# Performance work log

Measured on AMD Instinct MI355X. Metric: run time of the kernel, lower is better.

The kernel has to match this reference:

```python
import jax, jax.numpy as jnp
import numpy as np
from jax import lax

NPOL = 125   # polar grid size (hardcoded in module)
NANG = 126   # number of correlation offsets / angle bins


def polar_grid(n=NPOL):
    # u in [0, sqrt(2)], v in [-pi, pi]; torch.meshgrid default is 'ij'
    u = jnp.linspace(0.0, np.sqrt(2.0), n)
    v = jnp.linspace(-np.pi, np.pi, n)
    vs, us = jnp.meshgrid(v, u, indexing='ij')
    return jnp.stack([us * jnp.cos(vs), us * jnp.sin(vs)], axis=-1)  # (n, n, 2)


def grid_sample(img, grid):
    """Bilinear grid_sample, align_corners=True, zero padding.
    img: [B,C,H,W], grid: [B,Hg,Wg,2] (x,y) normalized coords. -> [B,C,Hg,Wg]"""
    B, C, H, W = img.shape
    ix = (grid[..., 0] + 1.0) * 0.5 * (W - 1)
    iy = (grid[..., 1] + 1.0) * 0.5 * (H - 1)
    x0 = jnp.floor(ix); y0 = jnp.floor(iy)
    x1 = x0 + 1.0; y1 = y0 + 1.0
    bidx = jnp.arange(B)[:, None, None]

    def corner(yc, xc, w):
        valid = (xc >= 0) & (xc <= W - 1) & (yc >= 0) & (yc <= H - 1)
        xi = jnp.clip(xc, 0, W - 1).astype(jnp.int32)
        yi = jnp.clip(yc, 0, H - 1).astype(jnp.int32)
        val = img[bidx, :, yi, xi]                 # [B,Hg,Wg,C]
        return val * (w * valid)[..., None]

    out = (corner(y0, x0, (x1 - ix) * (y1 - iy))
           + corner(y0, x1, (ix - x0) * (y1 - iy))
           + corner(y1, x0, (x1 - ix) * (iy - y0))
           + corner(y1, x1, (ix - x0) * (iy - y0)))
    return out.transpose(0, 3, 1, 2)


def affine_grid(mat, n=NPOL):
    # F.affine_grid align_corners=True over (n, n) output
    xs = jnp.linspace(-1.0, 1.0, n)
    yy, xx = jnp.meshgrid(xs, xs, indexing='ij')
    base = jnp.stack([xx, yy, jnp.ones_like(xx)], axis=-1)  # [n,n,3]
    return jnp.einsum('bij,hwj->bhwi', mat, base)           # [B,n,n,2]


def setup_inputs() -> dict:
    key = jax.random.key(0)
    k1, k2 = jax.random.split(key)
    Embd1 = jax.random.normal(k1, (32, 64, 128, 128), dtype=jnp.float32)
    Embd2 = jax.random.normal(k2, (32, 64, 128, 128), dtype=jnp.float32)
    return {"Embd1": Embd1, "Embd2": Embd2}


def reference(Embd1, Embd2):
    B, C, H, W = Embd1.shape
    pgrid = jnp.broadcast_to(polar_grid(), (B, NPOL, NPOL, 2))
    P1 = grid_sample(Embd1, pgrid)                 # [B,C,125,125]
    P2 = grid_sample(Embd2, pgrid)                 # [B,C,125,125]
    # torch.flip(input1, [1, 0]) flips channel AND batch dims (faithful)
    translated = jnp.flip(P1, axis=(0, 1))
    aug = jnp.concatenate([P1, translated], axis=2)  # [B,C,250,125]
    # per-sample full cross-correlation as grouped conv: 126 vertical offsets
    corr = lax.conv_general_dilated(
        aug.reshape(1, B * C, 2 * NPOL, NPOL), P2,
        window_strides=(1, 1), padding='VALID',
        dimension_numbers=('NCHW', 'OIHW', 'NCHW'),
        feature_group_count=B)                     # [1,B,126,1]
    scores = corr[0, :, :, 0]                      # [B,126]
    angles = jnp.linspace(-np.pi, np.pi, NANG)
    p = jax.nn.softmax(scores, axis=-1)
    theta = jnp.sum(p * angles, axis=-1) - np.pi   # [B]
    c, s = jnp.cos(theta), jnp.sin(theta)
    z = jnp.zeros_like(c)
    Mat = jnp.stack([jnp.stack([c, -s, z], axis=-1),
                     jnp.stack([s, c, z], axis=-1)], axis=1)  # [B,2,3]
    img_transform = grid_sample(Embd1, affine_grid(Mat))       # [B,C,125,125]
    return img_transform, Mat
```

## Files before the change

### kernel.cpp

```cpp
#include <hip/hip_runtime.h>
#include <math.h>
#include <stdint.h>

#define NPOL 125
#define NANG 126
#define BB 32
#define CC 64
#define HH 128
#define WW 128
#define PIX (NPOL*NPOL)
#define PI_F 3.14159265358979323846f

typedef __attribute__((ext_vector_type(4))) float f32x4;
typedef _Float16 f16x8 __attribute__((ext_vector_type(8)));
union U16 { uint4 u; f16x8 v; };

__global__ __launch_bounds__(256) void kz_zero(float* __restrict__ p, int n) {
    int i = blockIdx.x * 256 + threadIdx.x;
    if (i < n) p[i] = 0.0f;
}

__device__ __forceinline__ float bil(const float* __restrict__ img, float u, float cv, float sv) {
    float x = u * cv, y = u * sv;
    float ix = (x + 1.0f) * 0.5f * 127.0f;
    float iy = (y + 1.0f) * 0.5f * 127.0f;
    float x0 = floorf(ix), y0 = floorf(iy);
    float wx1 = ix - x0, wy1 = iy - y0;
    float wx0 = 1.0f - wx1, wy0 = 1.0f - wy1;
    float mx0 = (x0 >= 0.0f && x0 <= 127.0f) ? wx0 : 0.0f;
    float mx1 = (x0 >= -1.0f && x0 <= 126.0f) ? wx1 : 0.0f;
    float my0 = (y0 >= 0.0f && y0 <= 127.0f) ? wy0 : 0.0f;
    float my1 = (y0 >= -1.0f && y0 <= 126.0f) ? wy1 : 0.0f;
    int xi0 = (int)fminf(fmaxf(x0, 0.0f), 127.0f);
    int xi1 = (int)fminf(fmaxf(x0 + 1.0f, 0.0f), 127.0f);
    int yi0 = (int)fminf(fmaxf(y0, 0.0f), 127.0f);
    int yi1 = (int)fminf(fmaxf(y0 + 1.0f, 0.0f), 127.0f);
    return my0 * (mx0 * img[yi0 * WW + xi0] + mx1 * img[yi0 * WW + xi1])
         + my1 * (mx0 * img[yi1 * WW + xi0] + mx1 * img[yi1 * WW + xi1]);
}

__global__ __launch_bounds__(512, 2) void k2_fused(const float* __restrict__ E1,
                                                   const float* __restrict__ E2,
                                                   double* __restrict__ scores) {
    __shared__ unsigned bufA[16384];
    __shared__ unsigned bufB[16384];
    __shared__ float tabU[128];
    __shared__ float tabC[128];
    __shared__ float tabS[128];
    __shared__ double sd[2][NANG];

    const int tid  = threadIdx.x;
    const int lane = tid & 63;
    const int wid  = tid >> 6;
    const int wm   = wid >> 2;
    const int wn   = wid & 3;
    const int frow = lane & 15;
    const int kq   = lane >> 4;

    const int bp = blockIdx.x & 15;
    const int kg = blockIdx.x >> 4;

    if (tid < 128) {
        double dj = (double)tid;
        tabU[tid] = (tid < NPOL) ? (float)(dj * (1.4142135623730951 / 124.0)) : 0.0f;
        double v  = -3.14159265358979323846 + dj * (6.28318530717958647692 / 124.0);
        tabC[tid] = (tid < NPOL) ? (float)cos(v) : 0.0f;
        tabS[tid] = (tid < NPOL) ? (float)sin(v) : 0.0f;
    }
    if (tid < 2 * NANG) ((double*)sd)[tid] = 0.0;

    f32x4 acc0[4][2], acc1[4][2], acc2[4][2], acc3[4][2];
    #pragma unroll
    for (int mi = 0; mi < 4; ++mi)
        #pragma unroll
        for (int ni = 0; ni < 2; ++ni) {
            acc0[mi][ni] = (f32x4){0.f,0.f,0.f,0.f};
            acc1[mi][ni] = (f32x4){0.f,0.f,0.f,0.f};
            acc2[mi][ni] = (f32x4){0.f,0.f,0.f,0.f};
            acc3[mi][ni] = (f32x4){0.f,0.f,0.f,0.f};
        }

    float4 stg[8];
    unsigned hw[16], lw[16];

    {
        const float4* p0 = (const float4*)(E1 + (size_t)(bp * CC + kg * 4) * (HH * WW));
        #pragma unroll
        for (int k = 0; k < 8; ++k) stg[k] = p0[k * 512 + tid];
    }

#define LOADPLANE(BUF, NEXTP) do {                                              \
    _Pragma("unroll")                                                           \
    for (int k_ = 0; k_ < 8; ++k_) ((float4*)(BUF))[k_ * 512 + tid] = stg[k_];  \
    __syncthreads();                                                            \
    if (NEXTP) {                                                                \
        const float4* np_ = (const float4*)(NEXTP);                             \
        _Pragma("unroll")                                                       \
        for (int k_ = 0; k_ < 8; ++k_) stg[k_] = np_[k_ * 512 + tid];           \
    }                                                                           \
    {                                                                           \
        const float* f_ = (const float*)(BUF);                                  \
        _Pragma("unroll")                                                       \
        for (int it_ = 0; it_ < 16; ++it_) {                                    \
            int s_ = tid + it_ * 512;                                           \
            if (s_ < 8000) {                                                    \
                int r_ = s_ >> 6, p_ = s_ & 63;                                 \
                float cv_ = tabC[r_], sv_ = tabS[r_];                           \
                int j0_ = 2 * p_, j1_ = 2 * p_ + 1;                             \
                float va_ = bil(f_, tabU[j0_], cv_, sv_);                       \
                float vb_ = bil(f_, tabU[j1_], cv_, sv_);                       \
                if (j0_ >= NPOL) va_ = 0.0f;                                    \
                if (j1_ >= NPOL) vb_ = 0.0f;                                    \
                _Float16 h0_ = (_Float16)va_;                                   \
                _Float16 h1_ = (_Float16)vb_;                                   \
                _Float16 l0_ = (_Float16)(va_ - (float)h0_);                    \
                _Float16 l1_ = (_Float16)(vb_ - (float)h1_);                    \
                hw[it_] = (unsigned)__builtin_bit_cast(unsigned short, h0_)     \
                        | ((unsigned)__builtin_bit_cast(unsigned short, h1_) << 16); \
                lw[it_] = (unsigned)__builtin_bit_cast(unsigned short, l0_)     \
                        | ((unsigned)__builtin_bit_cast(unsigned short, l1_) << 16); \
            }                                                                   \
        }                                                                       \
    }                                                                           \
    __syncthreads();                                                            \
    _Pragma("unroll")                                                           \
    for (int it_ = 0; it_ < 16; ++it_) {                                        \
        int s_ = tid + it_ * 512;                                               \
        if (s_ < 8000) {                                                        \
            int r_ = s_ >> 6, p_ = s_ & 63;                                     \
            int ih_ = (r_ * 128 + p_) ^ ((r_ & 7) << 2);                        \
            (BUF)[ih_]      = hw[it_];                                          \
            (BUF)[ih_ + 64] = lw[it_];                                          \
        }                                                                       \
    }                                                                           \
    if (tid < 384) {                                                            \
        int rr_ = 125 + (tid >> 7), pp_ = tid & 127;                            \
        (BUF)[rr_ * 128 + pp_] = 0u;                                            \
    }                                                                           \
    __syncthreads();                                                            \
} while (0)

#define MPHASE(ACC) do {                                                        \
    _Pragma("unroll")                                                           \
    for (int jc_ = 0; jc_ < 4; ++jc_) {                                         \
        U16 ah_[4], al_[4], bh_[2], bl_[2];                                     \
        _Pragma("unroll")                                                       \
        for (int ni_ = 0; ni_ < 2; ++ni_) {                                     \
            int row_ = wn * 32 + ni_ * 16 + frow;                               \
            int idx_ = (row_ * 128 + jc_ * 16 + kq * 4) ^ ((row_ & 7) << 2);    \
            bh_[ni_].u = *(const uint4*)(bufB + idx_);                          \
            bl_[ni_].u = *(const uint4*)(bufB + idx_ + 64);                     \
        }                                                                       \
        _Pragma("unroll")                                                       \
        for (int mi_ = 0; mi_ < 4; ++mi_) {                                     \
            int row_ = wm * 64 + mi_ * 16 + frow;                               \
            int idx_ = (row_ * 128 + jc_ * 16 + kq * 4) ^ ((row_ & 7) << 2);    \
            ah_[mi_].u = *(const uint4*)(bufA + idx_);                          \
            al_[mi_].u = *(const uint4*)(bufA + idx_ + 64);                     \
        }                                                                       \
        _Pragma("unroll")                                                       \
        for (int mi_ = 0; mi_ < 4; ++mi_)                                       \
            _Pragma("unroll")                                                   \
            for (int ni_ = 0; ni_ < 2; ++ni_) {                                 \
                ACC[mi_][ni_] = __builtin_amdgcn_mfma_f32_16x16x32_f16(ah_[mi_].v, bh_[ni_].v, ACC[mi_][ni_], 0, 0, 0); \
                ACC[mi_][ni_] = __builtin_amdgcn_mfma_f32_16x16x32_f16(ah_[mi_].v, bl_[ni_].v, ACC[mi_][ni_], 0, 0, 0); \
                ACC[mi_][ni_] = __builtin_amdgcn_mfma_f32_16x16x32_f16(al_[mi_].v, bh_[ni_].v, ACC[mi_][ni_], 0, 0, 0); \
            }                                                                   \
    }                                                                           \
} while (0)

    for (int cl = 0; cl < 4; ++cl) {
        const int c  = kg * 4 + cl;
        const int cb = 63 - c;
        const float* pA1 = E1 + (size_t)(bp * CC + c) * (HH * WW);
        const float* pA2 = E1 + (size_t)((31 - bp) * CC + cb) * (HH * WW);
        const float* pB1 = E2 + (size_t)(bp * CC + c) * (HH * WW);
        const float* pB2 = E2 + (size_t)((31 - bp) * CC + cb) * (HH * WW);
        const float* pNx = (cl < 3) ? (pA1 + HH * WW) : nullptr;

        LOADPLANE(bufA, pB1);
        LOADPLANE(bufB, pA2);
        MPHASE(acc0);
        __syncthreads();
        LOADPLANE(bufA, pB2);
        MPHASE(acc1);
        __syncthreads();
        LOADPLANE(bufB, pA1);
        MPHASE(acc2);
        __syncthreads();
        LOADPLANE(bufA, pNx);
        MPHASE(acc3);
        __syncthreads();
    }

#define EPI(ACC, SDI, TOFF) do {                                                \
    float part_[5][4];                                                          \
    _Pragma("unroll")                                                           \
    for (int d_ = 0; d_ < 5; ++d_)                                              \
        _Pragma("unroll")                                                       \
        for (int r_ = 0; r_ < 4; ++r_) part_[d_][r_] = 0.0f;                    \
    _Pragma("unroll")                                                           \
    for (int mi_ = 0; mi_ < 4; ++mi_)                                           \
        _Pragma("unroll")                                                       \
        for (int ni_ = 0; ni_ < 2; ++ni_) {                                     \
            int d_ = mi_ - ni_ + 1;                                             \
            _Pragma("unroll")                                                   \
            for (int r_ = 0; r_ < 4; ++r_) part_[d_][r_] += ACC[mi_][ni_][r_];  \
        }                                                                       \
    int tb_ = (TOFF) + wm * 64 - wn * 32 + ((lane >> 4) << 2) - (lane & 15);    \
    _Pragma("unroll")                                                           \
    for (int d_ = 0; d_ < 5; ++d_)                                              \
        _Pragma("unroll")                                                       \
        for (int r_ = 0; r_ < 4; ++r_) {                                        \
            int t_ = tb_ + (d_ - 1) * 16 + r_;                                  \
            if (t_ >= 0 && t_ < NANG) atomicAdd(&sd[SDI][t_], (double)part_[d_][r_]); \
        }                                                                       \
} while (0)

    EPI(acc0, 0, 0);
    EPI(acc1, 0, 125);
    EPI(acc2, 1, 0);
    EPI(acc3, 1, 125);
    __syncthreads();
    if (tid < 2 * NANG) {
        int o = (tid < NANG) ? 0 : 1;
        int t = tid - o * NANG;
        int b = o ? (31 - bp) : bp;
        atomicAdd(&scores[b * NANG + t], sd[o][t]);
    }
#undef LOADPLANE
#undef MPHASE
#undef EPI
}

__global__ __launch_bounds__(128) void k3_theta(const double* __restrict__ scores, float* __restrict__ matOut) {
    const int b = blockIdx.x;
    const int t = threadIdx.x;
    __shared__ double sd[128];
    __shared__ double red[128];

    double sval = (t < NANG) ? scores[b * NANG + t] : -1e300;
    sd[t]  = sval;
    red[t] = sval;
    __syncthreads();
    for (int st = 64; st > 0; st >>= 1) {
        if (t < st) red[t] = fmax(red[t], red[t + st]);
        __syncthreads();
    }
    const double m = red[0];
    __syncthreads();
    const double e = (t < NANG) ? exp(sd[t] - m) : 0.0;
    red[t] = e;
    __syncthreads();
    for (int st = 64; st > 0; st >>= 1) {
        if (t < st) red[t] += red[t + st];
        __syncthreads();
    }
    const double Z = red[0];
    __syncthreads();
    const double ang = -3.14159265358979323846 + (double)t * (6.28318530717958647692 / 125.0);
    red[t] = e * ang;
    __syncthreads();
    for (int st = 64; st > 0; st >>= 1) {
        if (t < st) red[t] += red[t + st];
        __syncthreads();
    }
    if (t == 0) {
        double theta = red[0] / Z - 3.14159265358979323846;
        float cth = (float)cos(theta), sth = (float)sin(theta);
        float* M = matOut + b * 6;
        M[0] = cth; M[1] = -sth; M[2] = 0.0f;
        M[3] = sth; M[4] = cth;  M[5] = 0.0f;
    }
}

__global__ __launch_bounds__(512) void k4_affine(const float* __restrict__ img, const float* __restrict__ mat,
                                                 float* __restrict__ out) {
    __shared__ float plane[HH * WW];
    const int bc  = blockIdx.x;
    const int b   = bc >> 6;
    const int tid = threadIdx.x;
    const float4* src = (const float4*)img + (size_t)bc * (HH * WW / 4);
    float4* d4 = (float4*)plane;
    #pragma unroll
    for (int it = 0; it < 8; ++it) d4[it * 512 + tid] = src[it * 512 + tid];
    __syncthreads();
    const float M0 = mat[b * 6 + 0], M1 = mat[b * 6 + 1];
    const float M3 = mat[b * 6 + 3], M4 = mat[b * 6 + 4];
    const int base = bc * PIX;
    for (int pix = tid; pix < PIX; pix += 512) {
        int i = pix / NPOL;
        int j = pix - i * NPOL;
        float xx = (float)(-1.0 + (double)j * (2.0 / 124.0));
        float yy = (float)(-1.0 + (double)i * (2.0 / 124.0));
        float gx = M0 * xx + M1 * yy;
        float gy = M3 * xx + M4 * yy;
        float ix = (gx + 1.0f) * 0.5f * 127.0f;
        float iy = (gy + 1.0f) * 0.5f * 127.0f;
        float x0 = floorf(ix), y0 = floorf(iy);
        float wx1 = ix - x0, wy1 = iy - y0;
        float wx0 = 1.0f - wx1, wy0 = 1.0f - wy1;
        float mx0 = (x0 >= 0.0f && x0 <= 127.0f) ? wx0 : 0.0f;
        float mx1 = (x0 >= -1.0f && x0 <= 126.0f) ? wx1 : 0.0f;
        float my0 = (y0 >= 0.0f && y0 <= 127.0f) ? wy0 : 0.0f;
        float my1 = (y0 >= -1.0f && y0 <= 126.0f) ? wy1 : 0.0f;
        int xi0 = (int)fminf(fmaxf(x0, 0.0f), 127.0f);
        int xi1 = (int)fminf(fmaxf(x0 + 1.0f, 0.0f), 127.0f);
        int yi0 = (int)fminf(fmaxf(y0, 0.0f), 127.0f);
        int yi1 = (int)fminf(fmaxf(y0 + 1.0f, 0.0f), 127.0f);
        float val = my0 * (mx0 * plane[yi0 * WW + xi0] + mx1 * plane[yi0 * WW + xi1])
                  + my1 * (mx0 * plane[yi1 * WW + xi0] + mx1 * plane[yi1 * WW + xi1]);
        out[base + pix] = val;
    }
}

extern "C" void kernel_launch(void* const* d_in, const int* in_sizes, int n_in,
                              void* d_out, int out_size, void* d_ws, size_t ws_size,
                              hipStream_t stream) {
    const float* E1 = (const float*)d_in[0];
    const float* E2 = (const float*)d_in[1];
    float*  out    = (float*)d_out;
    float*  matOut = out + 32000000;
    double* scores = (double*)d_ws;

    kz_zero<<<(2 * BB * NANG + 255) / 256, 256, 0, stream>>>((float*)scores, 2 * BB * NANG);
    k2_fused<<<256, 512, 0, stream>>>(E1, E2, scores);
    k3_theta<<<BB, 128, 0, stream>>>(scores, matOut);
    k4_affine<<<BB * CC, 512, 0, stream>>>(E1, matOut, out);
}
```

Baseline: 420.0 us.

## Stage input planes with direct global-to-LDS loads instead of register prefetch

Replaces the register-staged prefetch, where the next plane was held in float4 registers while the current one was converted, with `global_load_lds` copies straight into shared memory. The load, convert and MFMA phases are reordered so each plane is staged, a barrier is taken, and then it is converted in place. The MFMA loop also loads A fragments one at a time instead of as a four-entry array. This frees many VGPRs, which may help occupancy and scheduling, but the next plane's global load no longer overlaps the current conversion, so load latency may be exposed at each barrier.

After: 621.9 us. +48.1%, slower.

```diff
diff --git a/kernel.cpp b/kernel.cpp
--- a/kernel.cpp
+++ b/kernel.cpp
@@ -18,6 +18,13 @@
 __global__ __launch_bounds__(256) void kz_zero(float* __restrict__ p, int n) {
     int i = blockIdx.x * 256 + threadIdx.x;
     if (i < n) p[i] = 0.0f;
+}
+
+__device__ __forceinline__ void gload16(const float* g, unsigned* l) {
+    __builtin_amdgcn_global_load_lds(
+        (const __attribute__((address_space(1))) void*)g,
+        (__attribute__((address_space(3))) void*)l,
+        16, 0, 0);
 }
 
 __device__ __forceinline__ float bil(const float* __restrict__ img, float u, float cv, float sv) {
@@ -80,46 +87,36 @@
             acc3[mi][ni] = (f32x4){0.f,0.f,0.f,0.f};
         }
 
-    float4 stg[8];
-    unsigned hw[16], lw[16];
-
-    {
-        const float4* p0 = (const float4*)(E1 + (size_t)(bp * CC + kg * 4) * (HH * WW));
-        #pragma unroll
-        for (int k = 0; k < 8; ++k) stg[k] = p0[k * 512 + tid];
-    }
-
-#define LOADPLANE(BUF, NEXTP) do {                                              \
-    _Pragma("unroll")                                                           \
-    for (int k_ = 0; k_ < 8; ++k_) ((float4*)(BUF))[k_ * 512 + tid] = stg[k_];  \
-    __syncthreads();                                                            \
-    if (NEXTP) {                                                                \
-        const float4* np_ = (const float4*)(NEXTP);                             \
-        _Pragma("unroll")                                                       \
-        for (int k_ = 0; k_ < 8; ++k_) stg[k_] = np_[k_ * 512 + tid];           \
-    }                                                                           \
-    {                                                                           \
-        const float* f_ = (const float*)(BUF);                                  \
-        _Pragma("unroll")                                                       \
-        for (int it_ = 0; it_ < 16; ++it_) {                                    \
-            int s_ = tid + it_ * 512;                                           \
-            if (s_ < 8000) {                                                    \
-                int r_ = s_ >> 6, p_ = s_ & 63;                                 \
-                float cv_ = tabC[r_], sv_ = tabS[r_];                           \
-                int j0_ = 2 * p_, j1_ = 2 * p_ + 1;                             \
-                float va_ = bil(f_, tabU[j0_], cv_, sv_);                       \
-                float vb_ = bil(f_, tabU[j1_], cv_, sv_);                       \
-                if (j0_ >= NPOL) va_ = 0.0f;                                    \
-                if (j1_ >= NPOL) vb_ = 0.0f;                                    \
-                _Float16 h0_ = (_Float16)va_;                                   \
-                _Float16 h1_ = (_Float16)vb_;                                   \
-                _Float16 l0_ = (_Float16)(va_ - (float)h0_);                    \
-                _Float16 l1_ = (_Float16)(vb_ - (float)h1_);                    \
-                hw[it_] = (unsigned)__builtin_bit_cast(unsigned short, h0_)     \
-                        | ((unsigned)__builtin_bit_cast(unsigned short, h1_) << 16); \
-                lw[it_] = (unsigned)__builtin_bit_cast(unsigned short, l0_)     \
-                        | ((unsigned)__builtin_bit_cast(unsigned short, l1_) << 16); \
-            }                                                                   \
+#define STAGE(BUF, PTR) do {                                                    \
+    const float* g_ = (PTR) + wid * 256 + lane * 4;                             \
+    unsigned* l_ = (BUF) + wid * 256;                                           \
+    _Pragma("unroll")                                                           \
+    for (int r_ = 0; r_ < 8; ++r_)                                              \
+        gload16(g_ + r_ * 2048, l_ + r_ * 2048);                                \
+} while (0)
+
+#define CONVERT(BUF) do {                                                       \
+    const float* f_ = (const float*)(BUF);                                      \
+    unsigned hw_[16], lw_[16];                                                  \
+    _Pragma("unroll")                                                           \
+    for (int it_ = 0; it_ < 16; ++it_) {                                        \
+        int s_ = tid + it_ * 512;                                               \
+        if (s_ < 8000) {                                                        \
+            int r_ = s_ >> 6, p_ = s_ & 63;                                     \
+            float cv_ = tabC[r_], sv_ = tabS[r_];                               \
+            int j0_ = 2 * p_, j1_ = 2 * p_ + 1;                                 \
+            float va_ = bil(f_, tabU[j0_], cv_, sv_);                           \
+            float vb_ = bil(f_, tabU[j1_], cv_, sv_);                           \
+            if (j0_ >= NPOL) va_ = 0.0f;                                        \
+            if (j1_ >= NPOL) vb_ = 0.0f;                                        \
+            _Float16 h0_ = (_Float16)va_;                                       \
+            _Float16 h1_ = (_Float16)vb_;                                       \
+            _Float16 l0_ = (_Float16)(va_ - (float)h0_);                        \
+            _Float16 l1_ = (_Float16)(vb_ - (float)h1_);                        \
+            hw_[it_] = (unsigned)__builtin_bit_cast(unsigned short, h0_)        \
+                     | ((unsigned)__builtin_bit_cast(unsigned short, h1_) << 16); \
+            lw_[it_] = (unsigned)__builtin_bit_cast(unsigned short, l0_)        \
+                     | ((unsigned)__builtin_bit_cast(unsigned short, l1_) << 16); \
         }                                                                       \
     }                                                                           \
     __syncthreads();                                                            \
@@ -129,8 +126,8 @@
         if (s_ < 8000) {                                                        \
             int r_ = s_ >> 6, p_ = s_ & 63;                                     \
             int ih_ = (r_ * 128 + p_) ^ ((r_ & 7) << 2);                        \
-            (BUF)[ih_]      = hw[it_];                                          \
-            (BUF)[ih_ + 64] = lw[it_];                                          \
+            (BUF)[ih_]      = hw_[it_];                                         \
+            (BUF)[ih_ + 64] = lw_[it_];                                         \
         }                                                                       \
     }                                                                           \
     if (tid < 384) {                                                            \
@@ -143,7 +140,7 @@
 #define MPHASE(ACC) do {                                                        \
     _Pragma("unroll")                                                           \
     for (int jc_ = 0; jc_ < 4; ++jc_) {                                         \
-        U16 ah_[4], al_[4], bh_[2], bl_[2];                                     \
+        U16 bh_[2], bl_[2];                                                     \
         _Pragma("unroll")                                                       \
         for (int ni_ = 0; ni_ < 2; ++ni_) {                                     \
             int row_ = wn * 32 + ni_ * 16 + frow;                               \
@@ -155,19 +152,25 @@
         for (int mi_ = 0; mi_ < 4; ++mi_) {                                     \
             int row_ = wm * 64 + mi_ * 16 + frow;                               \
             int idx_ = (row_ * 128 + jc_ * 16 + kq * 4) ^ ((row_ & 7) << 2);    \
-            ah_[mi_].u = *(const uint4*)(bufA + idx_);                          \
-            al_[mi_].u = *(const uint4*)(bufA + idx_ + 64);                     \
-        }                                                                       \
-        _Pragma("unroll")                                                       \
-        for (int mi_ = 0; mi_ < 4; ++mi_)                                       \
+            U16 ah_, al_;                                                       \
+            ah_.u = *(const uint4*)(bufA + idx_);                               \
+            al_.u = *(const uint4*)(bufA + idx_ + 64);                          \
             _Pragma("unroll")                                                   \
             for (int ni_ = 0; ni_ < 2; ++ni_) {                                 \
-                ACC[mi_][ni_] = __builtin_amdgcn_mfma_f32_16x16x32_f16(ah_[mi_].v, bh_[ni_].v, ACC[mi_][ni_], 0, 0, 0); \
-                ACC[mi_][ni_] = __builtin_amdgcn_mfma_f32_16x16x32_f16(ah_[mi_].v, bl_[ni_].v, ACC[mi_][ni_], 0, 0, 0); \
-                ACC[mi_][ni_] = __builtin_amdgcn_mfma_f32_16x16x32_f16(al_[mi_].v, bh_[ni_].v, ACC[mi_][ni_], 0, 0, 0); \
+                ACC[mi_][ni_] = __builtin_amdgcn_mfma_f32_16x16x32_f16(ah_.v, bh_[ni_].v, ACC[mi_][ni_], 0, 0, 0); \
+                ACC[mi_][ni_] = __builtin_amdgcn_mfma_f32_16x16x32_f16(ah_.v, bl_[ni_].v, ACC[mi_][ni_], 0, 0, 0); \
+                ACC[mi_][ni_] = __builtin_amdgcn_mfma_f32_16x16x32_f16(al_.v, bh_[ni_].v, ACC[mi_][ni_], 0, 0, 0); \
             }                                                                   \
+        }                                                                       \
     }                                                                           \
 } while (0)
+
+    {
+        const float* p0 = E1 + (size_t)(bp * CC + kg * 4) * (HH * WW);
+        const float* q0 = E2 + (size_t)(bp * CC + kg * 4) * (HH * WW);
+        STAGE(bufA, p0);
+        STAGE(bufB, q0);
+    }
 
     for (int cl = 0; cl < 4; ++cl) {
         const int c  = kg * 4 + cl;
@@ -176,21 +179,31 @@
         const float* pA2 = E1 + (size_t)((31 - bp) * CC + cb) * (HH * WW);
         const float* pB1 = E2 + (size_t)(bp * CC + c) * (HH * WW);
         const float* pB2 = E2 + (size_t)((31 - bp) * CC + cb) * (HH * WW);
-        const float* pNx = (cl < 3) ? (pA1 + HH * WW) : nullptr;
-
-        LOADPLANE(bufA, pB1);
-        LOADPLANE(bufB, pA2);
+
+        __syncthreads();
+        CONVERT(bufA);
+        CONVERT(bufB);
         MPHASE(acc0);
         __syncthreads();
-        LOADPLANE(bufA, pB2);
+        STAGE(bufA, pA2);
+        __syncthreads();
+        CONVERT(bufA);
         MPHASE(acc1);
         __syncthreads();
-        LOADPLANE(bufB, pA1);
+        STAGE(bufB, pB2);
+        __syncthreads();
+        CONVERT(bufB);
         MPHASE(acc2);
         __syncthreads();
-        LOADPLANE(bufA, pNx);
+        STAGE(bufA, pA1);
+        __syncthreads();
+        CONVERT(bufA);
         MPHASE(acc3);
-        __syncthreads();
+        if (cl < 3) {
+            __syncthreads();
+            STAGE(bufA, pA1 + HH * WW);
+            STAGE(bufB, pB1 + HH * WW);
+        }
     }
 
 #define EPI(ACC, SDI, TOFF) do {                                                \
@@ -217,6 +230,7 @@
         }                                                                       \
 } while (0)
 
+    __syncthreads();
     EPI(acc0, 0, 0);
     EPI(acc1, 0, 125);
     EPI(acc2, 1, 0);
@@ -228,7 +242,8 @@
         int b = o ? (31 - bp) : bp;
         atomicAdd(&scores[b * NANG + t], sd[o][t]);
     }
-#undef LOADPLANE
+#undef STAGE
+#undef CONVERT
 #undef MPHASE
 #undef EPI
 }
```
